# Kernel optimization log

Measured on AMD Instinct MI355X. Metric: run time of the kernel, lower is better.

Reference implementation:

```python
import jax, jax.numpy as jnp
import numpy as np

B, K, I, H, O = 256, 512, 64, 512, 1


def setup_inputs() -> dict:
    key = jax.random.key(0)
    ks = jax.random.split(key, 4)
    return {
        "input_seq": jax.random.normal(ks[0], (B, K, I), dtype=jnp.float32),
        "kernel": jax.random.normal(ks[1], (I, 4 * H), dtype=jnp.float32) * (2.0 / I) ** 0.5,
        "recurrent_kernel": jax.random.normal(ks[2], (4 * H, H), dtype=jnp.float32) * (2.0 / H) ** 0.5,
        "bias": jnp.zeros((4 * H,), dtype=jnp.float32),
        "Woutput": jax.random.normal(ks[3], (O, H), dtype=jnp.float32) * (2.0 / H) ** 0.5,
        "boutput": jnp.zeros((O,), dtype=jnp.float32),
    }


def reference(input_seq, kernel, recurrent_kernel, bias, Woutput, boutput):
    Bsz, Kt, _ = input_seq.shape
    Hs = recurrent_kernel.shape[1]
    # Precompute input projections for all timesteps: (K, B, 4H)
    x_proj = jnp.einsum("bki,ig->kbg", input_seq, kernel)

    def step(carry, x_t):
        h, c = carry
        # F.linear(h, recurrent_kernel, bias) == h @ recurrent_kernel.T + bias
        gates = x_t + h @ recurrent_kernel.T + bias  # (B, 4H)
        f_g, i_g, c_g, o_g = jnp.split(gates, 4, axis=1)
        f = jax.nn.sigmoid(f_g)
        i = jax.nn.sigmoid(i_g)
        c_prime = jnp.tanh(c_g)
        c_t = f * c + i * c_prime
        o = jax.nn.sigmoid(o_g)
        h_t = o * jnp.tanh(c_t)
        return (h_t, c_t), None

    h0 = jnp.zeros((Bsz, Hs), dtype=input_seq.dtype)
    c0 = jnp.zeros((Bsz, Hs), dtype=input_seq.dtype)
    (h_last, _), _ = jax.lax.scan(step, (h0, c0), x_proj)
    # Output layer applied to last timestep only (only lstm_out of final step is used)
    out = h_last @ Woutput.T + boutput  # (B, O)
    return out.reshape(-1)
```

## Files before the change

### kernel.cpp

```cpp
#include <hip/hip_runtime.h>

#define TSTEPS 512
#define BATCH  256
#define ISZ    64
#define HSZ    512
#define GSZ    2048
#define NKT    18
#define BG     16
#define ROWU   608
#define PLANE64 65536

typedef __attribute__((ext_vector_type(8))) short short8;
typedef __attribute__((ext_vector_type(4))) float f32x4;
typedef __attribute__((ext_vector_type(4))) unsigned int u32x4;
typedef unsigned long long u64t;

static __device__ __forceinline__ unsigned short f2bf(float f) {
    unsigned int u = __float_as_uint(f);
    return (unsigned short)((u + 0x7fffu + ((u >> 16) & 1u)) >> 16);
}
static __device__ __forceinline__ float sig_(float x) {
    return 1.0f / (1.0f + __expf(-x));
}
static __device__ __forceinline__ float tanh_(float x) {
    float e = __expf(-2.0f * fabsf(x));
    float t = (1.0f - e) / (1.0f + e);
    return copysignf(t, x);
}
static __device__ __forceinline__ u64t ld_tag64(const u64t* p) {
    return __hip_atomic_load(p, __ATOMIC_RELAXED, __HIP_MEMORY_SCOPE_AGENT);
}
static __device__ __forceinline__ void st_tag64(u64t* p, u64t v) {
    __hip_atomic_store(p, v, __ATOMIC_RELAXED, __HIP_MEMORY_SCOPE_AGENT);
}

__global__ void pack_w(const float* __restrict__ R, const float* __restrict__ Kin,
                       unsigned short* __restrict__ wpack)
{
    const int t  = blockIdx.x * 256 + threadIdx.x;
    const int l  = t & 63;
    const int kt = (t >> 6) % NKT;
    const int m  = (t / (64 * NKT)) & 7;
    const int jj = t / (64 * NKT * 8);
    const int r   = 16 * m + (l & 15);
    const int q   = r & 3;
    const int hco = r >> 2;
    const int grow  = q * HSZ + jj * 32 + hco;
    const int kbase = kt * 32 + (l >> 4) * 8;
    unsigned int pk[4];
#pragma unroll
    for (int p = 0; p < 4; ++p) {
        const int k0 = kbase + 2 * p;
        const int k1 = k0 + 1;
        const float f0 = (k0 < HSZ) ? R[(size_t)grow * HSZ + k0]
                                    : Kin[(size_t)(k0 - HSZ) * GSZ + grow];
        const float f1 = (k1 < HSZ) ? R[(size_t)grow * HSZ + k1]
                                    : Kin[(size_t)(k1 - HSZ) * GSZ + grow];
        pk[p] = (unsigned)f2bf(f0) | ((unsigned)f2bf(f1) << 16);
    }
    uint4 v = make_uint4(pk[0], pk[1], pk[2], pk[3]);
    *reinterpret_cast<uint4*>(wpack + (size_t)t * 8) = v;
}

__global__ void zero_tags(u32x4* __restrict__ hb) {
    u32x4 z = {0u, 0u, 0u, 0u};
    hb[blockIdx.x * 256 + threadIdx.x] = z;
}

__global__ __launch_bounds__(256, 1) void lstm_persist(
    const unsigned short* __restrict__ wpack,
    const float* __restrict__ input_seq,
    const float* __restrict__ bias,
    unsigned int* __restrict__ tbuf,
    float* __restrict__ hlast)
{
    __shared__ __align__(16) unsigned short lds_B[16][ROWU];
    __shared__ __align__(16) unsigned short lds_hn[16][40];
    const int tid = threadIdx.x;
    const int bid = blockIdx.x;
    const int gi = bid & 15;
    const int jw = bid >> 4;
    const int jj = jw;

    const int w  = tid >> 6;
    const int l  = tid & 63;
    const int bb = l & 15;
    const int lg = l >> 4;
    const int m0 = 2 * w, m1 = 2 * w + 1;

    short8 wA[NKT], wB[NKT];
#pragma unroll
    for (int kt = 0; kt < NKT; ++kt) {
        wA[kt] = *reinterpret_cast<const short8*>(
            wpack + (((size_t)(jj * 8 + m0) * NKT + kt) * 64 + l) * 8);
        wB[kt] = *reinterpret_cast<const short8*>(
            wpack + (((size_t)(jj * 8 + m1) * NKT + kt) * 64 + l) * 8);
    }
#pragma unroll
    for (int kt = 0; kt < NKT; ++kt) {
        asm volatile("" : "+a"(wA[kt]));
        asm volatile("" : "+a"(wB[kt]));
    }
    const int hc0 = 4 * m0 + lg, hc1 = 4 * m1 + lg;
    const int gh0 = jj * 32 + hc0, gh1 = jj * 32 + hc1;
    float bs0[4], bs1[4];
#pragma unroll
    for (int qg = 0; qg < 4; ++qg) {
        bs0[qg] = bias[qg * HSZ + gh0];
        bs1[qg] = bias[qg * HSZ + gh1];
    }

    float c0 = 0.f, c1 = 0.f;

    const int sb = tid & 15, sc = tid >> 4;
    const float* xbase = input_seq + (size_t)(gi * BG + sb) * (TSTEPS * ISZ) + sc * 4;
    float4 xr = *reinterpret_cast<const float4*>(xbase);

    const u64t* const hb0 = reinterpret_cast<const u64t*>(tbuf);
    const u64t* const hb1 = reinterpret_cast<const u64t*>(tbuf) + PLANE64;
    const int rr = tid >> 4, cch = tid & 15;
    const size_t csrc = (size_t)(gi * BG + rr) * 256 + cch;
    const int b_ = tid >> 4, pr = tid & 15;
    const size_t pdst = ((size_t)(gi * BG + b_) * HSZ + jw * 32 + pr * 2) >> 1;

    for (int s = 0; s < TSTEPS; ++s) {
        {
            uint2 px;
            px.x = (unsigned)f2bf(xr.x) | ((unsigned)f2bf(xr.y) << 16);
            px.y = (unsigned)f2bf(xr.z) | ((unsigned)f2bf(xr.w) << 16);
            *reinterpret_cast<uint2*>(&lds_B[sb][HSZ + sc * 4]) = px;
            if (s + 1 < TSTEPS)
                xr = *reinterpret_cast<const float4*>(xbase + (size_t)(s + 1) * ISZ);
        }
        if (s > 0) {
            const u64t* src = ((s & 1) ? hb1 : hb0) + csrc;
            const u64t want = ((u64t)(unsigned)s << 48) | ((u64t)(unsigned)s << 16);
            u64t v[16];
            bool ok;
            bool first = true;
            do {
                if (!first) __builtin_amdgcn_s_sleep(2);
                first = false;
                ok = true;
#pragma unroll
                for (int i = 0; i < 16; ++i)
                    v[i] = ld_tag64(src + (size_t)i * 16);
#pragma unroll
                for (int i = 0; i < 16; ++i)
                    ok = ok && ((v[i] & 0xFFFF0000FFFF0000ull) == want);
            } while (!ok);
#pragma unroll
            for (int i = 0; i < 16; ++i) {
                const unsigned d = (unsigned)(v[i] & 0xFFFFu) |
                                   ((unsigned)(v[i] >> 16) & 0xFFFF0000u);
                *reinterpret_cast<unsigned*>(&lds_B[rr][i * 32 + cch * 2]) = d;
            }
        } else {
#pragma unroll
            for (int i = 0; i < 16; ++i)
                *reinterpret_cast<unsigned*>(&lds_B[rr][i * 32 + cch * 2]) = 0u;
        }
        __syncthreads();

        f32x4 acc0 = {bs0[0], bs0[1], bs0[2], bs0[3]};
        f32x4 acc1 = {bs1[0], bs1[1], bs1[2], bs1[3]};
#pragma unroll
        for (int kt = 0; kt < NKT; ++kt) {
            const short8 bf = *reinterpret_cast<const short8*>(
                &lds_B[bb][kt * 32 + lg * 8]);
            acc0 = __builtin_amdgcn_mfma_f32_16x16x32_bf16(wA[kt], bf, acc0, 0, 0, 0);
            acc1 = __builtin_amdgcn_mfma_f32_16x16x32_bf16(wB[kt], bf, acc1, 0, 0, 0);
        }

        const float fg0 = sig_(acc0[0]);
        const float ig0 = sig_(acc0[1]);
        const float cp0 = tanh_(acc0[2]);
        const float og0 = sig_(acc0[3]);
        c0 = fg0 * c0 + ig0 * cp0;
        const float h0v = og0 * tanh_(c0);
        const float fg1 = sig_(acc1[0]);
        const float ig1 = sig_(acc1[1]);
        const float cp1 = tanh_(acc1[2]);
        const float og1 = sig_(acc1[3]);
        c1 = fg1 * c1 + ig1 * cp1;
        const float h1v = og1 * tanh_(c1);

        if (s == TSTEPS - 1) {
            hlast[(size_t)(gi * BG + bb) * HSZ + gh0] = h0v;
            hlast[(size_t)(gi * BG + bb) * HSZ + gh1] = h1v;
            break;
        }
        lds_hn[bb][hc0] = f2bf(h0v);
        lds_hn[bb][hc1] = f2bf(h1v);
        __syncthreads();

        {
            const unsigned h2 = *reinterpret_cast<const unsigned*>(&lds_hn[b_][pr * 2]);
            const unsigned t16 = (unsigned)(s + 1) << 16;
            const unsigned lo = (h2 & 0xFFFFu) | t16;
            const unsigned hi = (h2 >> 16) | t16;
            const u64t tagged = ((u64t)hi << 32) | (u64t)lo;
            u64t* dst = (u64t*)(tbuf) + (size_t)((s + 1) & 1) * PLANE64 + pdst;
            st_tag64(dst, tagged);
        }
    }
}

__global__ void out_kernel(const float* __restrict__ hlast,
                           const float* __restrict__ wout,
                           const float* __restrict__ bout,
                           float* __restrict__ out)
{
    const int b = blockIdx.x;
    const int l = threadIdx.x;
    float p = 0.f;
    for (int k = l; k < HSZ; k += 64)
        p += hlast[(size_t)b * HSZ + k] * wout[k];
    for (int off = 32; off > 0; off >>= 1)
        p += __shfl_down(p, off, 64);
    if (l == 0) out[b] = p + bout[0];
}

extern "C" void kernel_launch(void* const* d_in, const int* in_sizes, int n_in,
                              void* d_out, int out_size, void* d_ws, size_t ws_size,
                              hipStream_t stream) {
    const float* input_seq = (const float*)d_in[0];
    const float* Kin       = (const float*)d_in[1];
    const float* R         = (const float*)d_in[2];
    const float* bias      = (const float*)d_in[3];
    const float* Wout      = (const float*)d_in[4];
    const float* bout      = (const float*)d_in[5];
    float* out = (float*)d_out;

    char* ws = (char*)d_ws;
    unsigned short* wpack = (unsigned short*)(ws);
    unsigned int* tbuf    = (unsigned int*)(ws + 2359296);
    float* hlast          = (float*)(ws + 2359296 + 1048576);

    zero_tags<<<dim3(256), dim3(256), 0, stream>>>((u32x4*)tbuf);
    pack_w<<<dim3(576), dim3(256), 0, stream>>>(R, Kin, wpack);
    lstm_persist<<<dim3(256), dim3(256), 0, stream>>>(
        wpack, input_seq, bias, tbuf, hlast);
    out_kernel<<<dim3(256), dim3(64), 0, stream>>>(hlast, Wout, bout, out);
}
```

Before: 1.130 ms.

## Split each block into two independent half-blocks with per-half LDS barriers

```diff
diff --git a/kernel.cpp b/kernel.cpp
--- a/kernel.cpp
+++ b/kernel.cpp
@@ -74,35 +74,42 @@
     unsigned int* __restrict__ tbuf,
     float* __restrict__ hlast)
 {
-    __shared__ __align__(16) unsigned short lds_B[16][ROWU];
-    __shared__ __align__(16) unsigned short lds_hn[16][40];
+    __shared__ __align__(16) unsigned short lds_B[2][16][ROWU];
+    __shared__ __align__(16) unsigned short lds_hn[2][16][24];
+    __shared__ unsigned bcnt[2];
     const int tid = threadIdx.x;
     const int bid = blockIdx.x;
-    const int gi = bid & 15;
-    const int jw = bid >> 4;
-    const int jj = jw;
-
-    const int w  = tid >> 6;
+    const int p    = bid & 7;
+    const int sl   = bid >> 3;
+    const int w4   = tid >> 6;
+    const int half = w4 >> 1;
+    const int hw   = w4 & 1;
+    const int htid = tid & 127;
     const int l  = tid & 63;
     const int bb = l & 15;
     const int lg = l >> 4;
-    const int m0 = 2 * w, m1 = 2 * w + 1;
+    const int g  = p + 8 * half;
+
+    const int jjold = sl >> 1;
+    const int m0 = (sl & 1) * 4 + 2 * hw;
+    const int m1 = m0 + 1;
 
     short8 wA[NKT], wB[NKT];
 #pragma unroll
     for (int kt = 0; kt < NKT; ++kt) {
         wA[kt] = *reinterpret_cast<const short8*>(
-            wpack + (((size_t)(jj * 8 + m0) * NKT + kt) * 64 + l) * 8);
+            wpack + (((size_t)(jjold * 8 + m0) * NKT + kt) * 64 + l) * 8);
         wB[kt] = *reinterpret_cast<const short8*>(
-            wpack + (((size_t)(jj * 8 + m1) * NKT + kt) * 64 + l) * 8);
+            wpack + (((size_t)(jjold * 8 + m1) * NKT + kt) * 64 + l) * 8);
     }
 #pragma unroll
     for (int kt = 0; kt < NKT; ++kt) {
         asm volatile("" : "+a"(wA[kt]));
         asm volatile("" : "+a"(wB[kt]));
     }
-    const int hc0 = 4 * m0 + lg, hc1 = 4 * m1 + lg;
-    const int gh0 = jj * 32 + hc0, gh1 = jj * 32 + hc1;
+    const int lc0 = 8 * hw + lg;
+    const int lc1 = lc0 + 4;
+    const int gh0 = sl * 16 + lc0, gh1 = sl * 16 + lc1;
     float bs0[4], bs1[4];
 #pragma unroll
     for (int qg = 0; qg < 4; ++qg) {
@@ -112,62 +119,92 @@
 
     float c0 = 0.f, c1 = 0.f;
 
-    const int sb = tid & 15, sc = tid >> 4;
-    const float* xbase = input_seq + (size_t)(gi * BG + sb) * (TSTEPS * ISZ) + sc * 4;
-    float4 xr = *reinterpret_cast<const float4*>(xbase);
+    const int sb = htid & 15, sc2 = htid >> 4;
+    const float* xbase = input_seq + (size_t)(g * BG + sb) * (TSTEPS * ISZ) + sc2 * 8;
+    float4 xa = *reinterpret_cast<const float4*>(xbase);
+    float4 xc = *reinterpret_cast<const float4*>(xbase + 4);
 
     const u64t* const hb0 = reinterpret_cast<const u64t*>(tbuf);
     const u64t* const hb1 = reinterpret_cast<const u64t*>(tbuf) + PLANE64;
-    const int rr = tid >> 4, cch = tid & 15;
-    const size_t csrc = (size_t)(gi * BG + rr) * 256 + cch;
-    const int b_ = tid >> 4, pr = tid & 15;
-    const size_t pdst = ((size_t)(gi * BG + b_) * HSZ + jw * 32 + pr * 2) >> 1;
+    const int rr = htid >> 4, cch = htid & 15;
+    const int b_ = htid >> 3, pr = htid & 7;
+    const size_t pdst = (size_t)(g * BG + b_) * 256 + sl * 8 + pr;
+
+    if (tid < 2) bcnt[tid] = 0;
+    __syncthreads();
+    unsigned gen = 0;
+    volatile unsigned* bc = &bcnt[half];
+
+#define HBAR()                                                                 \
+    {                                                                          \
+        asm volatile("s_waitcnt lgkmcnt(0)" ::: "memory");                     \
+        ++gen;                                                                 \
+        if (l == 0)                                                            \
+            __hip_atomic_fetch_add((unsigned*)bc, 1u, __ATOMIC_RELAXED,        \
+                                   __HIP_MEMORY_SCOPE_WORKGROUP);              \
+        while (*bc < 2u * gen) { }                                             \
+        asm volatile("s_waitcnt lgkmcnt(0)" ::: "memory");                     \
+        __builtin_amdgcn_sched_barrier(0);                                     \
+    }
 
     for (int s = 0; s < TSTEPS; ++s) {
         {
-            uint2 px;
-            px.x = (unsigned)f2bf(xr.x) | ((unsigned)f2bf(xr.y) << 16);
-            px.y = (unsigned)f2bf(xr.z) | ((unsigned)f2bf(xr.w) << 16);
-            *reinterpret_cast<uint2*>(&lds_B[sb][HSZ + sc * 4]) = px;
-            if (s + 1 < TSTEPS)
-                xr = *reinterpret_cast<const float4*>(xbase + (size_t)(s + 1) * ISZ);
+            uint2 p0, p1;
+            p0.x = (unsigned)f2bf(xa.x) | ((unsigned)f2bf(xa.y) << 16);
+            p0.y = (unsigned)f2bf(xa.z) | ((unsigned)f2bf(xa.w) << 16);
+            p1.x = (unsigned)f2bf(xc.x) | ((unsigned)f2bf(xc.y) << 16);
+            p1.y = (unsigned)f2bf(xc.z) | ((unsigned)f2bf(xc.w) << 16);
+            *reinterpret_cast<uint2*>(&lds_B[half][sb][HSZ + sc2 * 8]) = p0;
+            *reinterpret_cast<uint2*>(&lds_B[half][sb][HSZ + sc2 * 8 + 4]) = p1;
+            if (s + 1 < TSTEPS) {
+                xa = *reinterpret_cast<const float4*>(xbase + (size_t)(s + 1) * ISZ);
+                xc = *reinterpret_cast<const float4*>(xbase + (size_t)(s + 1) * ISZ + 4);
+            }
         }
         if (s > 0) {
-            const u64t* src = ((s & 1) ? hb1 : hb0) + csrc;
+            const u64t* plane = (s & 1) ? hb1 : hb0;
             const u64t want = ((u64t)(unsigned)s << 48) | ((u64t)(unsigned)s << 16);
-            u64t v[16];
-            bool ok;
-            bool first = true;
-            do {
-                if (!first) __builtin_amdgcn_s_sleep(2);
-                first = false;
-                ok = true;
-#pragma unroll
-                for (int i = 0; i < 16; ++i)
-                    v[i] = ld_tag64(src + (size_t)i * 16);
-#pragma unroll
-                for (int i = 0; i < 16; ++i)
-                    ok = ok && ((v[i] & 0xFFFF0000FFFF0000ull) == want);
-            } while (!ok);
-#pragma unroll
-            for (int i = 0; i < 16; ++i) {
-                const unsigned d = (unsigned)(v[i] & 0xFFFFu) |
-                                   ((unsigned)(v[i] >> 16) & 0xFFFF0000u);
-                *reinterpret_cast<unsigned*>(&lds_B[rr][i * 32 + cch * 2]) = d;
+#pragma unroll
+            for (int j = 0; j < 2; ++j) {
+                const int row = rr + 8 * j;
+                const u64t* src = plane + (size_t)(g * BG + row) * 256 + cch;
+                u64t v[16];
+                bool ok;
+                bool first = true;
+                do {
+                    if (!first) __builtin_amdgcn_s_sleep(2);
+                    first = false;
+                    ok = true;
+#pragma unroll
+                    for (int i = 0; i < 16; ++i)
+                        v[i] = ld_tag64(src + (size_t)i * 16);
+#pragma unroll
+                    for (int i = 0; i < 16; ++i)
+                        ok = ok && ((v[i] & 0xFFFF0000FFFF0000ull) == want);
+                } while (!ok);
+#pragma unroll
+                for (int i = 0; i < 16; ++i) {
+                    const unsigned d = (unsigned)(v[i] & 0xFFFFu) |
+                                       ((unsigned)(v[i] >> 16) & 0xFFFF0000u);
+                    *reinterpret_cast<unsigned*>(&lds_B[half][row][i * 32 + cch * 2]) = d;
+                }
             }
         } else {
 #pragma unroll
-            for (int i = 0; i < 16; ++i)
-                *reinterpret_cast<unsigned*>(&lds_B[rr][i * 32 + cch * 2]) = 0u;
-        }
-        __syncthreads();
+            for (int j = 0; j < 2; ++j)
+#pragma unroll
+                for (int i = 0; i < 16; ++i)
+                    *reinterpret_cast<unsigned*>(
+                        &lds_B[half][rr + 8 * j][i * 32 + cch * 2]) = 0u;
+        }
+        HBAR();
 
         f32x4 acc0 = {bs0[0], bs0[1], bs0[2], bs0[3]};
         f32x4 acc1 = {bs1[0], bs1[1], bs1[2], bs1[3]};
 #pragma unroll
         for (int kt = 0; kt < NKT; ++kt) {
             const short8 bf = *reinterpret_cast<const short8*>(
-                &lds_B[bb][kt * 32 + lg * 8]);
+                &lds_B[half][bb][kt * 32 + lg * 8]);
             acc0 = __builtin_amdgcn_mfma_f32_16x16x32_bf16(wA[kt], bf, acc0, 0, 0, 0);
             acc1 = __builtin_amdgcn_mfma_f32_16x16x32_bf16(wB[kt], bf, acc1, 0, 0, 0);
         }
@@ -186,16 +223,17 @@
         const float h1v = og1 * tanh_(c1);
 
         if (s == TSTEPS - 1) {
-            hlast[(size_t)(gi * BG + bb) * HSZ + gh0] = h0v;
-            hlast[(size_t)(gi * BG + bb) * HSZ + gh1] = h1v;
+            hlast[(size_t)(g * BG + bb) * HSZ + gh0] = h0v;
+            hlast[(size_t)(g * BG + bb) * HSZ + gh1] = h1v;
             break;
         }
-        lds_hn[bb][hc0] = f2bf(h0v);
-        lds_hn[bb][hc1] = f2bf(h1v);
-        __syncthreads();
+        lds_hn[half][bb][lc0] = f2bf(h0v);
+        lds_hn[half][bb][lc1] = f2bf(h1v);
+        HBAR();
 
         {
-            const unsigned h2 = *reinterpret_cast<const unsigned*>(&lds_hn[b_][pr * 2]);
+            const unsigned h2 = *reinterpret_cast<const unsigned*>(
+                &lds_hn[half][b_][pr * 2]);
             const unsigned t16 = (unsigned)(s + 1) << 16;
             const unsigned lo = (h2 & 0xFFFFu) | t16;
             const unsigned hi = (h2 >> 16) | t16;
@@ -204,6 +242,7 @@
             st_tag64(dst, tagged);
         }
     }
+#undef HBAR
 }
 
 __global__ void out_kernel(const float* __restrict__ hlast,
```

Result: slower. 1.453 ms (+28.6%).

## Replace LDS staging barrier with wave bpermute and double-buffer LDS input tile

Applied to the files above, without the earlier changes.

```diff
diff --git a/kernel.cpp b/kernel.cpp
--- a/kernel.cpp
+++ b/kernel.cpp
@@ -74,8 +74,7 @@
     unsigned int* __restrict__ tbuf,
     float* __restrict__ hlast)
 {
-    __shared__ __align__(16) unsigned short lds_B[16][ROWU];
-    __shared__ __align__(16) unsigned short lds_hn[16][40];
+    __shared__ __align__(16) unsigned short lds_B[2][16][ROWU];
     const int tid = threadIdx.x;
     const int bid = blockIdx.x;
     const int gi = bid & 15;
@@ -120,15 +119,20 @@
     const u64t* const hb1 = reinterpret_cast<const u64t*>(tbuf) + PLANE64;
     const int rr = tid >> 4, cch = tid & 15;
     const size_t csrc = (size_t)(gi * BG + rr) * 256 + cch;
-    const int b_ = tid >> 4, pr = tid & 15;
-    const size_t pdst = ((size_t)(gi * BG + b_) * HSZ + jw * 32 + pr * 2) >> 1;
+    const int pb = l >> 2, pp = l & 3;
+    const size_t pdst = (size_t)(gi * BG + pb) * 256 + jw * 16 + 4 * w + pp;
+    const int lgs = (pp & 1) * 2;
+    const int idx1 = (((lgs) << 4) | pb) << 2;
+    const int idx2 = (((lgs + 1) << 4) | pb) << 2;
+    const bool hiHalf = (pp >= 2);
 
     for (int s = 0; s < TSTEPS; ++s) {
+        const int pl = s & 1;
         {
             uint2 px;
             px.x = (unsigned)f2bf(xr.x) | ((unsigned)f2bf(xr.y) << 16);
             px.y = (unsigned)f2bf(xr.z) | ((unsigned)f2bf(xr.w) << 16);
-            *reinterpret_cast<uint2*>(&lds_B[sb][HSZ + sc * 4]) = px;
+            *reinterpret_cast<uint2*>(&lds_B[pl][sb][HSZ + sc * 4]) = px;
             if (s + 1 < TSTEPS)
                 xr = *reinterpret_cast<const float4*>(xbase + (size_t)(s + 1) * ISZ);
         }
@@ -153,12 +157,12 @@
             for (int i = 0; i < 16; ++i) {
                 const unsigned d = (unsigned)(v[i] & 0xFFFFu) |
                                    ((unsigned)(v[i] >> 16) & 0xFFFF0000u);
-                *reinterpret_cast<unsigned*>(&lds_B[rr][i * 32 + cch * 2]) = d;
+                *reinterpret_cast<unsigned*>(&lds_B[pl][rr][i * 32 + cch * 2]) = d;
             }
         } else {
 #pragma unroll
             for (int i = 0; i < 16; ++i)
-                *reinterpret_cast<unsigned*>(&lds_B[rr][i * 32 + cch * 2]) = 0u;
+                *reinterpret_cast<unsigned*>(&lds_B[pl][rr][i * 32 + cch * 2]) = 0u;
         }
         __syncthreads();
 
@@ -167,7 +171,7 @@
 #pragma unroll
         for (int kt = 0; kt < NKT; ++kt) {
             const short8 bf = *reinterpret_cast<const short8*>(
-                &lds_B[bb][kt * 32 + lg * 8]);
+                &lds_B[pl][bb][kt * 32 + lg * 8]);
             acc0 = __builtin_amdgcn_mfma_f32_16x16x32_bf16(wA[kt], bf, acc0, 0, 0, 0);
             acc1 = __builtin_amdgcn_mfma_f32_16x16x32_bf16(wB[kt], bf, acc1, 0, 0, 0);
         }
@@ -190,16 +194,15 @@
             hlast[(size_t)(gi * BG + bb) * HSZ + gh1] = h1v;
             break;
         }
-        lds_hn[bb][hc0] = f2bf(h0v);
-        lds_hn[bb][hc1] = f2bf(h1v);
-        __syncthreads();
 
         {
-            const unsigned h2 = *reinterpret_cast<const unsigned*>(&lds_hn[b_][pr * 2]);
+            const unsigned pk = (unsigned)f2bf(h0v) | ((unsigned)f2bf(h1v) << 16);
+            const unsigned r1 = (unsigned)__builtin_amdgcn_ds_bpermute(idx1, (int)pk);
+            const unsigned r2 = (unsigned)__builtin_amdgcn_ds_bpermute(idx2, (int)pk);
+            const unsigned val1 = hiHalf ? (r1 >> 16) : (r1 & 0xFFFFu);
+            const unsigned val2 = hiHalf ? (r2 >> 16) : (r2 & 0xFFFFu);
             const unsigned t16 = (unsigned)(s + 1) << 16;
-            const unsigned lo = (h2 & 0xFFFFu) | t16;
-            const unsigned hi = (h2 >> 16) | t16;
-            const u64t tagged = ((u64t)hi << 32) | (u64t)lo;
+            const u64t tagged = ((u64t)(val2 | t16) << 32) | (u64t)(val1 | t16);
             u64t* dst = (u64t*)(tbuf) + (size_t)((s + 1) & 1) * PLANE64 + pdst;
             st_tag64(dst, tagged);
         }
```

Result: slower. 1.176 ms (+4.1%).
